# Performance work log

Hardware: AMD Instinct MI355X
Metric: run time of the kernel (lower is better)

Reference implementation:

```python
import jax, jax.numpy as jnp
import numpy as np

EPS_BN = 1e-5   # torch BatchNorm1d default eps
EPS_L1 = 1e-9   # offset-attention renorm eps


def batchnorm(x, g, b):
    # training-mode BN over (batch, points) per channel; x: [B, C, N]
    mu = x.mean(axis=(0, 2), keepdims=True)
    var = x.var(axis=(0, 2), keepdims=True)  # biased, matching torch normalization
    return g[None, :, None] * (x - mu) * jax.lax.rsqrt(var + EPS_BN) + b[None, :, None]


def sub_ie(x, Wqk, Wv, bv, Wt, bt, g, b):
    # x: [B, C, N]; Wqk: [C//4, C] (q_conv and k_conv share weights)
    q = jnp.einsum('dc,bcn->bdn', Wqk, x)                    # [B, C/4, N]
    energy = jnp.einsum('bdi,bdj->bij', q, q)                # [B, N, N] symmetric Gram
    att = jax.nn.softmax(energy, axis=-1)                    # softmax over keys (dim=-1)
    att = att / (EPS_L1 + att.sum(axis=1, keepdims=True))    # extra L1 renorm over queries (dim=1)
    v = jnp.einsum('dc,bcn->bdn', Wv, x) + bv[None, :, None]  # [B, C, N]
    x_r = jnp.einsum('bci,bij->bcj', v, att)                 # bmm(x_v, attention)
    y = jnp.einsum('dc,bcn->bdn', Wt, x - x_r) + bt[None, :, None]
    y = jax.nn.relu(batchnorm(y, g, b))
    return x + y


def setup_inputs() -> dict:
    key = jax.random.key(0)
    ks = jax.random.split(key, 8)
    B, Cin, C, N = 8, 64, 128, 2048
    s = lambda k, shape: jax.random.normal(k, shape, jnp.float32) * 0.05
    return {
        'x':   jax.random.normal(ks[0], (B, Cin, N), jnp.float32),
        'W1':  s(ks[1], (64, 64)),
        'g1':  jnp.ones(64, jnp.float32),  'b1': jnp.zeros(64, jnp.float32),
        'W2':  s(ks[2], (C, 64)),
        'g2':  jnp.ones(C, jnp.float32),   'b2': jnp.zeros(C, jnp.float32),
        'Wqk': s(ks[3], (4, C // 4, C)),
        'Wv':  s(ks[4], (4, C, C)),        'bv': jnp.zeros((4, C), jnp.float32),
        'Wt':  s(ks[5], (4, C, C)),        'bt': jnp.zeros((4, C), jnp.float32),
        'gn':  jnp.ones((4, C), jnp.float32), 'bnb': jnp.zeros((4, C), jnp.float32),
    }


def reference(x, W1, g1, b1, W2, g2, b2, Wqk, Wv, bv, Wt, bt, gn, bnb):
    h = jax.nn.relu(batchnorm(jnp.einsum('dc,bcn->bdn', W1, x), g1, b1))   # [B,64,N]
    h = jax.nn.relu(batchnorm(jnp.einsum('dc,bcn->bdn', W2, h), g2, b2))   # [B,128,N]
    outs = []
    for i in range(4):  # 4 structurally chained offset-attention blocks
        h = sub_ie(h, Wqk[i], Wv[i], bv[i], Wt[i], bt[i], gn[i], bnb[i])
        outs.append(h)
    return jnp.concatenate(outs, axis=1)  # [B, 512, N]
```

## Files before the change

### kernel.cpp

```cpp
#include <hip/hip_runtime.h>
#include <cstdint>
#include <cstddef>

#define NPTS 2048
#define NBAT 8

typedef unsigned long long ull;
typedef __attribute__((ext_vector_type(8))) short bf16x8;
typedef __attribute__((ext_vector_type(4))) float f32x4;

__device__ __forceinline__ float4 ld4(const float* p){ return *reinterpret_cast<const float4*>(p); }
__device__ __forceinline__ void st4(float* p, float4 v){ *reinterpret_cast<float4*>(p) = v; }
__device__ __forceinline__ unsigned short f2bf(float f){
    unsigned int u = __float_as_uint(f);
    u += 0x7FFFu + ((u >> 16) & 1u);
    return (unsigned short)(u >> 16);
}
__device__ __forceinline__ float bf2f(unsigned short h){
    return __uint_as_float(((unsigned int)h) << 16);
}

#define BAR_LDS() do { asm volatile("s_waitcnt lgkmcnt(0)" ::: "memory"); \
                       __builtin_amdgcn_s_barrier(); } while (0)

__global__ __launch_bounds__(256) void zero_kernel(float* __restrict__ p)
{
    int i = (blockIdx.x * 256 + threadIdx.x) * 4;
    st4(&p[i], (float4){0.f, 0.f, 0.f, 0.f});
}

__device__ __forceinline__ void bn_finalize(const float* part, int C, int c,
                                            float& mean, float& istd)
{
    float s = 0.f, s2 = 0.f;
    #pragma unroll
    for (int b = 0; b < NBAT; ++b) {
        s  += part[b * C + c];
        s2 += part[NBAT * C + b * C + c];
    }
    const float invn = 1.f / (NBAT * NPTS);
    mean = s * invn;
    float var = s2 * invn - mean * mean;
    istd = rsqrtf(var + 1e-5f);
}

template<int CIN, int COUT, int TD, int TN, int MODE, bool BIAS, bool BNIN, bool STATS>
__global__ __launch_bounds__(256) void lin_mfma_kernel(
        const float* __restrict__ W, const float* __restrict__ X,
        const float* __restrict__ bias,
        const float* __restrict__ gin, const float* __restrict__ betain,
        const float* __restrict__ pin, float* __restrict__ pout,
        void* __restrict__ outv, void* __restrict__ outv2)
{
    constexpr int WD  = TD / 16;
    constexpr int NPW = TN * WD / 4;
    constexpr int FB  = NPW / 16;
    constexpr int KS  = CIN / 32;
    __shared__ unsigned short Xhi[TN * CIN];
    __shared__ unsigned short Xlo[TN * CIN];
    __shared__ float gaL[CIN];
    __shared__ float beL[CIN];
    const int tid = threadIdx.x;
    const int lane = tid & 63;
    const int w = tid >> 6;
    const int g = lane >> 4;
    const int l15 = lane & 15;
    const int b = blockIdx.z;
    const int d0 = blockIdx.y * TD;
    const int n0 = blockIdx.x * TN;
    const int dw = (w % WD) * 16;
    const int nw = (w / WD) * NPW;

    if (BNIN) {
        if (tid < CIN) {
            float mean, is;
            bn_finalize(pin, CIN, tid, mean, is);
            float ga = gin[tid] * is;
            gaL[tid] = ga;
            beL[tid] = betain[tid] - mean * ga;
        }
        __syncthreads();
    }

    bf16x8 Whi[KS], Wlo[KS];
    {
        const int d = d0 + dw + l15;
        #pragma unroll
        for (int ks = 0; ks < KS; ++ks) {
            float4 a = ld4(&W[(size_t)d * CIN + ks * 32 + g * 8]);
            float4 bq = ld4(&W[(size_t)d * CIN + ks * 32 + g * 8 + 4]);
            float vv[8] = {a.x, a.y, a.z, a.w, bq.x, bq.y, bq.z, bq.w};
            bf16x8 h8, l8;
            #pragma unroll
            for (int e = 0; e < 8; ++e) {
                unsigned short hh = f2bf(vv[e]);
                h8[e] = (short)hh;
                l8[e] = (short)f2bf(vv[e] - bf2f(hh));
            }
            Whi[ks] = h8; Wlo[ks] = l8;
        }
    }
    constexpr int TN4 = TN / 4;
    constexpr int NF = (TN * CIN) / 1024;
    #pragma unroll
    for (int f = 0; f < NF; ++f) {
        int idx = tid + 256 * f;
        int c = idx / TN4;
        int n = (idx % TN4) * 4;
        float4 xv = ld4(&X[((size_t)(b * CIN + c)) * NPTS + n0 + n]);
        float vv[4] = {xv.x, xv.y, xv.z, xv.w};
        if (BNIN) {
            float ga = gaL[c], be = beL[c];
            #pragma unroll
            for (int j2 = 0; j2 < 4; ++j2) vv[j2] = fmaxf(fmaf(ga, vv[j2], be), 0.f);
        }
        #pragma unroll
        for (int j2 = 0; j2 < 4; ++j2) {
            int nn = n + j2;
            int cp = (c + nn * 8) & (CIN - 1);
            unsigned short hh = f2bf(vv[j2]);
            Xhi[nn * CIN + cp] = hh;
            Xlo[nn * CIN + cp] = f2bf(vv[j2] - bf2f(hh));
        }
    }
    __syncthreads();

    f32x4 acc[FB];
    #pragma unroll
    for (int fb = 0; fb < FB; ++fb) acc[fb] = (f32x4){0.f, 0.f, 0.f, 0.f};
    #pragma unroll
    for (int ks = 0; ks < KS; ++ks) {
        #pragma unroll
        for (int fb = 0; fb < FB; ++fb) {
            int n = nw + fb * 16 + l15;
            int cp = (ks * 32 + g * 8 + n * 8) & (CIN - 1);
            bf16x8 xh = *reinterpret_cast<bf16x8*>(&Xhi[n * CIN + cp]);
            bf16x8 xl = *reinterpret_cast<bf16x8*>(&Xlo[n * CIN + cp]);
            acc[fb] = __builtin_amdgcn_mfma_f32_16x16x32_bf16(Wlo[ks], xh, acc[fb], 0, 0, 0);
            acc[fb] = __builtin_amdgcn_mfma_f32_16x16x32_bf16(Whi[ks], xl, acc[fb], 0, 0, 0);
            acc[fb] = __builtin_amdgcn_mfma_f32_16x16x32_bf16(Whi[ks], xh, acc[fb], 0, 0, 0);
        }
    }
    const int dbase = d0 + dw + g * 4;
    float bb[4] = {0.f, 0.f, 0.f, 0.f};
    if (BIAS) {
        float4 b4 = ld4(&bias[dbase]);
        bb[0] = b4.x; bb[1] = b4.y; bb[2] = b4.z; bb[3] = b4.w;
    }
    float s1[4] = {0.f, 0.f, 0.f, 0.f};
    float s2[4] = {0.f, 0.f, 0.f, 0.f};
    #pragma unroll
    for (int fb = 0; fb < FB; ++fb) {
        int ncol = n0 + nw + fb * 16 + l15;
        if (MODE == 2) {
            unsigned short* qh = (unsigned short*)outv;
            unsigned short* ql = (unsigned short*)outv2;
            ushort4 hh, ll;
            float q0 = acc[fb][0], q1 = acc[fb][1], q2 = acc[fb][2], q3 = acc[fb][3];
            hh.x = f2bf(q0); ll.x = f2bf(q0 - bf2f(hh.x));
            hh.y = f2bf(q1); ll.y = f2bf(q1 - bf2f(hh.y));
            hh.z = f2bf(q2); ll.z = f2bf(q2 - bf2f(hh.z));
            hh.w = f2bf(q3); ll.w = f2bf(q3 - bf2f(hh.w));
            *reinterpret_cast<ushort4*>(&qh[((size_t)b * NPTS + ncol) * 32 + dbase]) = hh;
            *reinterpret_cast<ushort4*>(&ql[((size_t)b * NPTS + ncol) * 32 + dbase]) = ll;
        } else if (MODE == 1) {
            unsigned short* ob = (unsigned short*)outv;
            #pragma unroll
            for (int r = 0; r < 4; ++r)
                ob[((size_t)(b * COUT + dbase + r)) * NPTS + ncol] = f2bf(acc[fb][r] + bb[r]);
        } else {
            float* ob = (float*)outv;
            #pragma unroll
            for (int r = 0; r < 4; ++r) {
                float val = acc[fb][r] + bb[r];
                ob[((size_t)(b * COUT + dbase + r)) * NPTS + ncol] = val;
                if (STATS) { s1[r] += val; s2[r] += val * val; }
            }
        }
    }
    if (STATS) {
        #pragma unroll
        for (int r = 0; r < 4; ++r) {
            float a1 = s1[r], a2 = s2[r];
            a1 += __shfl_xor(a1, 1, 64);  a2 += __shfl_xor(a2, 1, 64);
            a1 += __shfl_xor(a1, 2, 64);  a2 += __shfl_xor(a2, 2, 64);
            a1 += __shfl_xor(a1, 4, 64);  a2 += __shfl_xor(a2, 4, 64);
            a1 += __shfl_xor(a1, 8, 64);  a2 += __shfl_xor(a2, 8, 64);
            if (l15 == 0) {
                atomicAdd(&pout[b * COUT + dbase + r], a1);
                atomicAdd(&pout[NBAT * COUT + b * COUT + dbase + r], a2);
            }
        }
    }
}

__global__ __launch_bounds__(256) void rowstats_fused_kernel(
        const unsigned short* __restrict__ qThi, const unsigned short* __restrict__ qTlo,
        float* __restrict__ rowm, float* __restrict__ rowinv)
{
    __shared__ float pm[4][32];
    __shared__ float ps[4][32];
    const int tid = threadIdx.x;
    const int lane = tid & 63;
    const int w = tid >> 6;
    const int b = blockIdx.y;
    const int i0 = blockIdx.x * 32;
    const int g = lane >> 4;
    const int l15 = lane & 15;
    const bf16x8 b0h = *reinterpret_cast<const bf16x8*>(&qThi[((size_t)b * NPTS + i0 + l15) * 32 + g * 8]);
    const bf16x8 b0l = *reinterpret_cast<const bf16x8*>(&qTlo[((size_t)b * NPTS + i0 + l15) * 32 + g * 8]);
    const bf16x8 b1h = *reinterpret_cast<const bf16x8*>(&qThi[((size_t)b * NPTS + i0 + 16 + l15) * 32 + g * 8]);
    const bf16x8 b1l = *reinterpret_cast<const bf16x8*>(&qTlo[((size_t)b * NPTS + i0 + 16 + l15) * 32 + g * 8]);
    float m0 = -1e30f, s0 = 0.f, m1 = -1e30f, s1 = 0.f;
    for (int t = w * 32; t < w * 32 + 32; ++t) {
        int jr = t * 16 + l15;
        const bf16x8 ahi = *reinterpret_cast<const bf16x8*>(&qThi[((size_t)b * NPTS + jr) * 32 + g * 8]);
        const bf16x8 alo = *reinterpret_cast<const bf16x8*>(&qTlo[((size_t)b * NPTS + jr) * 32 + g * 8]);
        f32x4 e0 = {0.f, 0.f, 0.f, 0.f};
        e0 = __builtin_amdgcn_mfma_f32_16x16x32_bf16(alo, b0h, e0, 0, 0, 0);
        e0 = __builtin_amdgcn_mfma_f32_16x16x32_bf16(ahi, b0l, e0, 0, 0, 0);
        e0 = __builtin_amdgcn_mfma_f32_16x16x32_bf16(ahi, b0h, e0, 0, 0, 0);
        f32x4 e1 = {0.f, 0.f, 0.f, 0.f};
        e1 = __builtin_amdgcn_mfma_f32_16x16x32_bf16(alo, b1h, e1, 0, 0, 0);
        e1 = __builtin_amdgcn_mfma_f32_16x16x32_bf16(ahi, b1l, e1, 0, 0, 0);
        e1 = __builtin_amdgcn_mfma_f32_16x16x32_bf16(ahi, b1h, e1, 0, 0, 0);
        float tm0 = fmaxf(fmaxf(e0[0], e0[1]), fmaxf(e0[2], e0[3]));
        float nm0 = fmaxf(m0, tm0);
        s0 *= __expf(m0 - nm0);
        m0 = nm0;
        s0 += __expf(e0[0] - m0) + __expf(e0[1] - m0) + __expf(e0[2] - m0) + __expf(e0[3] - m0);
        float tm1 = fmaxf(fmaxf(e1[0], e1[1]), fmaxf(e1[2], e1[3]));
        float nm1 = fmaxf(m1, tm1);
        s1 *= __expf(m1 - nm1);
        m1 = nm1;
        s1 += __expf(e1[0] - m1) + __expf(e1[1] - m1) + __expf(e1[2] - m1) + __expf(e1[3] - m1);
    }
    #pragma unroll
    for (int o = 16; o <= 32; o <<= 1) {
        float om = __shfl_xor(m0, o, 64);
        float os = __shfl_xor(s0, o, 64);
        float nm = fmaxf(m0, om);
        s0 = s0 * __expf(m0 - nm) + os * __expf(om - nm);
        m0 = nm;
        om = __shfl_xor(m1, o, 64);
        os = __shfl_xor(s1, o, 64);
        nm = fmaxf(m1, om);
        s1 = s1 * __expf(m1 - nm) + os * __expf(om - nm);
        m1 = nm;
    }
    if (lane < 16) {
        pm[w][l15] = m0; ps[w][l15] = s0;
        pm[w][16 + l15] = m1; ps[w][16 + l15] = s1;
    }
    __syncthreads();
    if (tid < 32) {
        float ma = pm[0][tid], mb = pm[1][tid], mc = pm[2][tid], md = pm[3][tid];
        float mf = fmaxf(fmaxf(ma, mb), fmaxf(mc, md));
        float sf = ps[0][tid] * __expf(ma - mf) + ps[1][tid] * __expf(mb - mf)
                 + ps[2][tid] * __expf(mc - mf) + ps[3][tid] * __expf(md - mf);
        rowm[(size_t)b * NPTS + i0 + tid] = mf;
        rowinv[(size_t)b * NPTS + i0 + tid] = 1.f / sf;
    }
}

__global__ __launch_bounds__(512) void attn_fused_kernel(
        const unsigned short* __restrict__ qThi, const unsigned short* __restrict__ qTlo,
        const unsigned short* __restrict__ V,
        const float* __restrict__ rowm, const float* __restrict__ rowinv,
        const float* __restrict__ H, float* __restrict__ T)
{
    __shared__ unsigned short Alds[2][128 * 64];
    __shared__ unsigned short Blds[2][32 * 64];
    __shared__ float cparts[8][16];
    const int tid = threadIdx.x;
    const int b  = blockIdx.y;
    const int j0 = blockIdx.x * 32;
    const int lane = tid & 63;
    const int w = tid >> 6;
    const int g = lane >> 4;
    const int l15 = lane & 15;
    const int jsub = w & 1;
    const int tE = w >> 1;
    const int jl = jsub * 16 + l15;
    const int cb = (w >> 1) * 32;
    const int jb = jsub * 16;
    const int vc = tid >> 3, vslot = tid & 7;
    const int vc1 = (tid + 512) >> 3, vslot1 = (tid + 512) & 7;
    const bf16x8 bhi = *reinterpret_cast<const bf16x8*>(&qThi[((size_t)b * NPTS + j0 + jl) * 32 + g * 8]);
    const bf16x8 blo = *reinterpret_cast<const bf16x8*>(&qTlo[((size_t)b * NPTS + j0 + jl) * 32 + g * 8]);
    f32x4 acc[2];
    acc[0] = (f32x4){0.f, 0.f, 0.f, 0.f};
    acc[1] = (f32x4){0.f, 0.f, 0.f, 0.f};
    float csum = 0.f;

    float4 vreg0 = ld4((const float*)(V + ((size_t)(b * 128 + vc)) * NPTS + vslot * 8));
    float4 vreg1 = ld4((const float*)(V + ((size_t)(b * 128 + vc1)) * NPTS + vslot1 * 8));
    bf16x8 pahi = *reinterpret_cast<const bf16x8*>(&qThi[((size_t)b * NPTS + tE * 16 + l15) * 32 + g * 8]);
    bf16x8 palo = *reinterpret_cast<const bf16x8*>(&qTlo[((size_t)b * NPTS + tE * 16 + l15) * 32 + g * 8]);
    float4 pmv = ld4(&rowm[(size_t)b * NPTS + tE * 16 + g * 4]);
    float4 psv = ld4(&rowinv[(size_t)b * NPTS + tE * 16 + g * 4]);

    int p = 0;
    for (int i0 = 0; i0 < NPTS; i0 += 64) {
        {
            int sl = vslot ^ (vc & 7);
            *reinterpret_cast<float4*>(&Alds[p][vc * 64 + sl * 8]) = vreg0;
            sl = vslot1 ^ (vc1 & 7);
            *reinterpret_cast<float4*>(&Alds[p][vc1 * 64 + sl * 8]) = vreg1;
        }
        {
            f32x4 e4 = {0.f, 0.f, 0.f, 0.f};
            __builtin_amdgcn_s_setprio(1);
            e4 = __builtin_amdgcn_mfma_f32_16x16x32_bf16(palo, bhi, e4, 0, 0, 0);
            e4 = __builtin_amdgcn_mfma_f32_16x16x32_bf16(pahi, blo, e4, 0, 0, 0);
            e4 = __builtin_amdgcn_mfma_f32_16x16x32_bf16(pahi, bhi, e4, 0, 0, 0);
            __builtin_amdgcn_s_setprio(0);
            float p0 = __expf(e4[0] - pmv.x) * psv.x;
            float p1 = __expf(e4[1] - pmv.y) * psv.y;
            float p2 = __expf(e4[2] - pmv.z) * psv.z;
            float p3 = __expf(e4[3] - pmv.w) * psv.w;
            csum += p0 + p1 + p2 + p3;
            int il = tE * 16 + g * 4;
            int sl = (il >> 3) ^ (jl & 7);
            ull pk = (ull)f2bf(p0) | ((ull)f2bf(p1) << 16) |
                     ((ull)f2bf(p2) << 32) | ((ull)f2bf(p3) << 48);
            *reinterpret_cast<ull*>(&Blds[p][jl * 64 + sl * 8 + (il & 7)]) = pk;
        }
        {
            int i0n = (i0 + 64) & (NPTS - 1);
            vreg0 = ld4((const float*)(V + ((size_t)(b * 128 + vc)) * NPTS + i0n + vslot * 8));
            vreg1 = ld4((const float*)(V + ((size_t)(b * 128 + vc1)) * NPTS + i0n + vslot1 * 8));
            pahi = *reinterpret_cast<const bf16x8*>(&qThi[((size_t)b * NPTS + i0n + tE * 16 + l15) * 32 + g * 8]);
            palo = *reinterpret_cast<const bf16x8*>(&qTlo[((size_t)b * NPTS + i0n + tE * 16 + l15) * 32 + g * 8]);
            pmv = ld4(&rowm[(size_t)b * NPTS + i0n + tE * 16 + g * 4]);
            psv = ld4(&rowinv[(size_t)b * NPTS + i0n + tE * 16 + g * 4]);
        }
        BAR_LDS();
        __builtin_amdgcn_s_setprio(1);
        #pragma unroll
        for (int ks = 0; ks < 2; ++ks) {
            int j = jb + l15;
            int slb = (ks * 4 + g) ^ (j & 7);
            bf16x8 bfr = *reinterpret_cast<bf16x8*>(&Blds[p][j * 64 + slb * 8]);
            #pragma unroll
            for (int fa = 0; fa < 2; ++fa) {
                int c = cb + fa * 16 + l15;
                int sla = (ks * 4 + g) ^ (c & 7);
                bf16x8 afr = *reinterpret_cast<bf16x8*>(&Alds[p][c * 64 + sla * 8]);
                acc[fa] = __builtin_amdgcn_mfma_f32_16x16x32_bf16(afr, bfr, acc[fa], 0, 0, 0);
            }
        }
        __builtin_amdgcn_s_setprio(0);
        p ^= 1;
    }
    csum += __shfl_xor(csum, 16, 64);
    csum += __shfl_xor(csum, 32, 64);
    if (lane < 16) cparts[w][l15] = csum;
    __syncthreads();
    float cs = cparts[jsub][l15] + cparts[jsub + 2][l15]
             + cparts[jsub + 4][l15] + cparts[jsub + 6][l15];
    float inv = 1.f / (1e-9f + cs);
    int jg_ = j0 + jb + l15;
    #pragma unroll
    for (int fa = 0; fa < 2; ++fa) {
        #pragma unroll
        for (int r = 0; r < 4; ++r) {
            int c = cb + fa * 16 + g * 4 + r;
            size_t base = ((size_t)(b * 128 + c)) * NPTS + jg_;
            T[base] = H[base] - acc[fa][r] * inv;
        }
    }
}

__global__ __launch_bounds__(256) void bn_apply_kernel(const float* __restrict__ X,
        const float* __restrict__ g, const float* __restrict__ beta,
        const float* __restrict__ part, int C, float* __restrict__ out)
{
    const int bc = blockIdx.y;
    const int c = bc % C;
    const int n = blockIdx.x * 1024 + threadIdx.x * 4;
    float mean, is;
    bn_finalize(part, C, c, mean, is);
    const float ga = g[c] * is;
    const float be = beta[c] - mean * ga;
    float4 v = ld4(&X[(size_t)bc * NPTS + n]);
    float4 o;
    o.x = fmaxf(fmaf(ga, v.x, be), 0.f);
    o.y = fmaxf(fmaf(ga, v.y, be), 0.f);
    o.z = fmaxf(fmaf(ga, v.z, be), 0.f);
    o.w = fmaxf(fmaf(ga, v.w, be), 0.f);
    st4(&out[(size_t)bc * NPTS + n], o);
}

__global__ __launch_bounds__(256) void bn_res_kernel(const float* __restrict__ Y,
        const float* __restrict__ g, const float* __restrict__ beta,
        const float* __restrict__ part, float* __restrict__ H,
        float* __restrict__ out, int blk)
{
    const int bc = blockIdx.y;
    const int c = bc & 127;
    const int b = bc >> 7;
    const int n = blockIdx.x * 1024 + threadIdx.x * 4;
    float mean, is;
    bn_finalize(part, 128, c, mean, is);
    const float ga = g[c] * is;
    const float be = beta[c] - mean * ga;
    float4 yv = ld4(&Y[(size_t)bc * NPTS + n]);
    float4 hv = ld4(&H[(size_t)bc * NPTS + n]);
    float4 o;
    o.x = hv.x + fmaxf(fmaf(ga, yv.x, be), 0.f);
    o.y = hv.y + fmaxf(fmaf(ga, yv.y, be), 0.f);
    o.z = hv.z + fmaxf(fmaf(ga, yv.z, be), 0.f);
    o.w = hv.w + fmaxf(fmaf(ga, yv.w, be), 0.f);
    st4(&H[(size_t)bc * NPTS + n], o);
    st4(&out[((size_t)(b * 512 + blk * 128 + c)) * NPTS + n], o);
}

extern "C" void kernel_launch(void* const* d_in, const int* in_sizes, int n_in,
                              void* d_out, int out_size, void* d_ws, size_t ws_size,
                              hipStream_t stream)
{
    const float* x   = (const float*)d_in[0];
    const float* W1  = (const float*)d_in[1];
    const float* g1  = (const float*)d_in[2];
    const float* b1  = (const float*)d_in[3];
    const float* W2  = (const float*)d_in[4];
    const float* g2  = (const float*)d_in[5];
    const float* b2  = (const float*)d_in[6];
    const float* Wqk = (const float*)d_in[7];
    const float* Wv  = (const float*)d_in[8];
    const float* bv  = (const float*)d_in[9];
    const float* Wt  = (const float*)d_in[10];
    const float* bt  = (const float*)d_in[11];
    const float* gn  = (const float*)d_in[12];
    const float* bnb = (const float*)d_in[13];
    float* out = (float*)d_out;

    float* ws = (float*)d_ws;
    size_t off = 0;
    auto alloc = [&](size_t n) { float* p = ws + off; off += n; return p; };
    float* h      = alloc((size_t)NBAT * 128 * NPTS);
    float* t      = alloc((size_t)NBAT * 128 * NPTS);
    float* y      = alloc((size_t)NBAT * 128 * NPTS);
    float* y2     = alloc((size_t)NBAT * 128 * NPTS);
    float* part   = alloc(6 * 2 * NBAT * 128);
    float* rowm   = alloc((size_t)NBAT * NPTS);
    float* rowinv = alloc((size_t)NBAT * NPTS);
    unsigned short* vb   = (unsigned short*)alloc((size_t)NBAT * 128 * NPTS / 2);
    unsigned short* qThi = (unsigned short*)alloc((size_t)NBAT * NPTS * 32 / 2);
    unsigned short* qTlo = (unsigned short*)alloc((size_t)NBAT * NPTS * 32 / 2);
    const int PSL = 2 * NBAT * 128;

    zero_kernel<<<12, 256, 0, stream>>>(part);

    lin_mfma_kernel<64, 64, 64, 32, 0, false, false, true>
        <<<dim3(64, 1, NBAT), 256, 0, stream>>>(
        W1, x, nullptr, nullptr, nullptr, nullptr, part + 0 * PSL, y, nullptr);
    lin_mfma_kernel<64, 128, 64, 32, 0, false, true, true>
        <<<dim3(64, 2, NBAT), 256, 0, stream>>>(
        W2, y, nullptr, g1, b1, part + 0 * PSL, part + 1 * PSL, y2, nullptr);
    bn_apply_kernel<<<dim3(2, NBAT * 128), 256, 0, stream>>>(
        y2, g2, b2, part + 1 * PSL, 128, h);

    for (int blk = 0; blk < 4; ++blk) {
        lin_mfma_kernel<128, 32, 32, 32, 2, false, false, false>
            <<<dim3(64, 1, NBAT), 256, 0, stream>>>(
            Wqk + (size_t)blk * 32 * 128, h, nullptr,
            nullptr, nullptr, nullptr, nullptr, qThi, qTlo);
        lin_mfma_kernel<128, 128, 64, 32, 1, true, false, false>
            <<<dim3(64, 2, NBAT), 256, 0, stream>>>(
            Wv + (size_t)blk * 128 * 128, h, bv + blk * 128,
            nullptr, nullptr, nullptr, nullptr, vb, nullptr);
        rowstats_fused_kernel<<<dim3(64, NBAT), 256, 0, stream>>>(qThi, qTlo, rowm, rowinv);
        attn_fused_kernel<<<dim3(64, NBAT), 512, 0, stream>>>(
            qThi, qTlo, vb, rowm, rowinv, h, t);
        lin_mfma_kernel<128, 128, 64, 32, 0, true, false, true>
            <<<dim3(64, 2, NBAT), 256, 0, stream>>>(
            Wt + (size_t)blk * 128 * 128, t, bt + blk * 128,
            nullptr, nullptr, nullptr, part + (2 + blk) * PSL, y, nullptr);
        bn_res_kernel<<<dim3(2, NBAT * 128), 256, 0, stream>>>(
            y, gn + blk * 128, bnb + blk * 128, part + (2 + blk) * PSL, h, out, blk);
    }
}
```

Before: 409.7 us.

## Load V tiles via global_load_lds, widen attention K-step, shrink rowstats tile

```diff
diff --git a/kernel.cpp b/kernel.cpp
--- a/kernel.cpp
+++ b/kernel.cpp
@@ -20,8 +20,11 @@
     return __uint_as_float(((unsigned int)h) << 16);
 }
 
-#define BAR_LDS() do { asm volatile("s_waitcnt lgkmcnt(0)" ::: "memory"); \
-                       __builtin_amdgcn_s_barrier(); } while (0)
+typedef __attribute__((address_space(3))) unsigned int lds_u32;
+typedef __attribute__((address_space(1))) const unsigned int glb_u32;
+__device__ __forceinline__ void gl2lds16(const unsigned short* g, unsigned short* l){
+    __builtin_amdgcn_global_load_lds((glb_u32*)g, (lds_u32*)l, 16, 0, 0);
+}
 
 __global__ __launch_bounds__(256) void zero_kernel(float* __restrict__ p)
 {
@@ -198,68 +201,52 @@
         const unsigned short* __restrict__ qThi, const unsigned short* __restrict__ qTlo,
         float* __restrict__ rowm, float* __restrict__ rowinv)
 {
-    __shared__ float pm[4][32];
-    __shared__ float ps[4][32];
-    const int tid = threadIdx.x;
-    const int lane = tid & 63;
-    const int w = tid >> 6;
+    __shared__ float pm[4][16];
+    __shared__ float ps[4][16];
+    const int lane = threadIdx.x & 63;
+    const int w = threadIdx.x >> 6;
     const int b = blockIdx.y;
-    const int i0 = blockIdx.x * 32;
+    const int i0 = blockIdx.x * 16;
     const int g = lane >> 4;
     const int l15 = lane & 15;
-    const bf16x8 b0h = *reinterpret_cast<const bf16x8*>(&qThi[((size_t)b * NPTS + i0 + l15) * 32 + g * 8]);
-    const bf16x8 b0l = *reinterpret_cast<const bf16x8*>(&qTlo[((size_t)b * NPTS + i0 + l15) * 32 + g * 8]);
-    const bf16x8 b1h = *reinterpret_cast<const bf16x8*>(&qThi[((size_t)b * NPTS + i0 + 16 + l15) * 32 + g * 8]);
-    const bf16x8 b1l = *reinterpret_cast<const bf16x8*>(&qTlo[((size_t)b * NPTS + i0 + 16 + l15) * 32 + g * 8]);
-    float m0 = -1e30f, s0 = 0.f, m1 = -1e30f, s1 = 0.f;
+    const int iR = i0 + l15;
+    const bf16x8 bhi = *reinterpret_cast<const bf16x8*>(&qThi[((size_t)b * NPTS + iR) * 32 + g * 8]);
+    const bf16x8 blo = *reinterpret_cast<const bf16x8*>(&qTlo[((size_t)b * NPTS + iR) * 32 + g * 8]);
+    float m = -1e30f, s = 0.f;
     for (int t = w * 32; t < w * 32 + 32; ++t) {
         int jr = t * 16 + l15;
         const bf16x8 ahi = *reinterpret_cast<const bf16x8*>(&qThi[((size_t)b * NPTS + jr) * 32 + g * 8]);
         const bf16x8 alo = *reinterpret_cast<const bf16x8*>(&qTlo[((size_t)b * NPTS + jr) * 32 + g * 8]);
-        f32x4 e0 = {0.f, 0.f, 0.f, 0.f};
-        e0 = __builtin_amdgcn_mfma_f32_16x16x32_bf16(alo, b0h, e0, 0, 0, 0);
-        e0 = __builtin_amdgcn_mfma_f32_16x16x32_bf16(ahi, b0l, e0, 0, 0, 0);
-        e0 = __builtin_amdgcn_mfma_f32_16x16x32_bf16(ahi, b0h, e0, 0, 0, 0);
-        f32x4 e1 = {0.f, 0.f, 0.f, 0.f};
-        e1 = __builtin_amdgcn_mfma_f32_16x16x32_bf16(alo, b1h, e1, 0, 0, 0);
-        e1 = __builtin_amdgcn_mfma_f32_16x16x32_bf16(ahi, b1l, e1, 0, 0, 0);
-        e1 = __builtin_amdgcn_mfma_f32_16x16x32_bf16(ahi, b1h, e1, 0, 0, 0);
-        float tm0 = fmaxf(fmaxf(e0[0], e0[1]), fmaxf(e0[2], e0[3]));
-        float nm0 = fmaxf(m0, tm0);
-        s0 *= __expf(m0 - nm0);
-        m0 = nm0;
-        s0 += __expf(e0[0] - m0) + __expf(e0[1] - m0) + __expf(e0[2] - m0) + __expf(e0[3] - m0);
-        float tm1 = fmaxf(fmaxf(e1[0], e1[1]), fmaxf(e1[2], e1[3]));
-        float nm1 = fmaxf(m1, tm1);
-        s1 *= __expf(m1 - nm1);
-        m1 = nm1;
-        s1 += __expf(e1[0] - m1) + __expf(e1[1] - m1) + __expf(e1[2] - m1) + __expf(e1[3] - m1);
+        f32x4 e4 = {0.f, 0.f, 0.f, 0.f};
+        e4 = __builtin_amdgcn_mfma_f32_16x16x32_bf16(alo, bhi, e4, 0, 0, 0);
+        e4 = __builtin_amdgcn_mfma_f32_16x16x32_bf16(ahi, blo, e4, 0, 0, 0);
+        e4 = __builtin_amdgcn_mfma_f32_16x16x32_bf16(ahi, bhi, e4, 0, 0, 0);
+        float tm = fmaxf(fmaxf(e4[0], e4[1]), fmaxf(e4[2], e4[3]));
+        float nm = fmaxf(m, tm);
+        s *= __expf(m - nm);
+        m = nm;
+        s += __expf(e4[0] - m) + __expf(e4[1] - m) + __expf(e4[2] - m) + __expf(e4[3] - m);
     }
     #pragma unroll
     for (int o = 16; o <= 32; o <<= 1) {
-        float om = __shfl_xor(m0, o, 64);
-        float os = __shfl_xor(s0, o, 64);
-        float nm = fmaxf(m0, om);
-        s0 = s0 * __expf(m0 - nm) + os * __expf(om - nm);
-        m0 = nm;
-        om = __shfl_xor(m1, o, 64);
-        os = __shfl_xor(s1, o, 64);
-        nm = fmaxf(m1, om);
-        s1 = s1 * __expf(m1 - nm) + os * __expf(om - nm);
-        m1 = nm;
-    }
-    if (lane < 16) {
-        pm[w][l15] = m0; ps[w][l15] = s0;
-        pm[w][16 + l15] = m1; ps[w][16 + l15] = s1;
-    }
+        float om = __shfl_xor(m, o, 64);
+        float os = __shfl_xor(s, o, 64);
+        float nm = fmaxf(m, om);
+        s = s * __expf(m - nm) + os * __expf(om - nm);
+        m = nm;
+    }
+    if (lane < 16) { pm[w][l15] = m; ps[w][l15] = s; }
     __syncthreads();
-    if (tid < 32) {
-        float ma = pm[0][tid], mb = pm[1][tid], mc = pm[2][tid], md = pm[3][tid];
-        float mf = fmaxf(fmaxf(ma, mb), fmaxf(mc, md));
-        float sf = ps[0][tid] * __expf(ma - mf) + ps[1][tid] * __expf(mb - mf)
-                 + ps[2][tid] * __expf(mc - mf) + ps[3][tid] * __expf(md - mf);
-        rowm[(size_t)b * NPTS + i0 + tid] = mf;
-        rowinv[(size_t)b * NPTS + i0 + tid] = 1.f / sf;
+    if (threadIdx.x < 16) {
+        float m0 = pm[0][threadIdx.x], m1 = pm[1][threadIdx.x];
+        float m2 = pm[2][threadIdx.x], m3 = pm[3][threadIdx.x];
+        float mf = fmaxf(fmaxf(m0, m1), fmaxf(m2, m3));
+        float sf = ps[0][threadIdx.x] * __expf(m0 - mf)
+                 + ps[1][threadIdx.x] * __expf(m1 - mf)
+                 + ps[2][threadIdx.x] * __expf(m2 - mf)
+                 + ps[3][threadIdx.x] * __expf(m3 - mf);
+        rowm[(size_t)b * NPTS + i0 + threadIdx.x] = mf;
+        rowinv[(size_t)b * NPTS + i0 + threadIdx.x] = 1.f / sf;
     }
 }
 
@@ -269,8 +256,8 @@
         const float* __restrict__ rowm, const float* __restrict__ rowinv,
         const float* __restrict__ H, float* __restrict__ T)
 {
-    __shared__ unsigned short Alds[2][128 * 64];
-    __shared__ unsigned short Blds[2][32 * 64];
+    __shared__ unsigned short Alds[128 * 128];
+    __shared__ unsigned short Blds[32 * 128];
     __shared__ float cparts[8][16];
     const int tid = threadIdx.x;
     const int b  = blockIdx.y;
@@ -280,12 +267,9 @@
     const int g = lane >> 4;
     const int l15 = lane & 15;
     const int jsub = w & 1;
-    const int tE = w >> 1;
     const int jl = jsub * 16 + l15;
     const int cb = (w >> 1) * 32;
     const int jb = jsub * 16;
-    const int vc = tid >> 3, vslot = tid & 7;
-    const int vc1 = (tid + 512) >> 3, vslot1 = (tid + 512) & 7;
     const bf16x8 bhi = *reinterpret_cast<const bf16x8*>(&qThi[((size_t)b * NPTS + j0 + jl) * 32 + g * 8]);
     const bf16x8 blo = *reinterpret_cast<const bf16x8*>(&qTlo[((size_t)b * NPTS + j0 + jl) * 32 + g * 8]);
     f32x4 acc[2];
@@ -293,65 +277,56 @@
     acc[1] = (f32x4){0.f, 0.f, 0.f, 0.f};
     float csum = 0.f;
 
-    float4 vreg0 = ld4((const float*)(V + ((size_t)(b * 128 + vc)) * NPTS + vslot * 8));
-    float4 vreg1 = ld4((const float*)(V + ((size_t)(b * 128 + vc1)) * NPTS + vslot1 * 8));
-    bf16x8 pahi = *reinterpret_cast<const bf16x8*>(&qThi[((size_t)b * NPTS + tE * 16 + l15) * 32 + g * 8]);
-    bf16x8 palo = *reinterpret_cast<const bf16x8*>(&qTlo[((size_t)b * NPTS + tE * 16 + l15) * 32 + g * 8]);
-    float4 pmv = ld4(&rowm[(size_t)b * NPTS + tE * 16 + g * 4]);
-    float4 psv = ld4(&rowinv[(size_t)b * NPTS + tE * 16 + g * 4]);
-
-    int p = 0;
-    for (int i0 = 0; i0 < NPTS; i0 += 64) {
-        {
-            int sl = vslot ^ (vc & 7);
-            *reinterpret_cast<float4*>(&Alds[p][vc * 64 + sl * 8]) = vreg0;
-            sl = vslot1 ^ (vc1 & 7);
-            *reinterpret_cast<float4*>(&Alds[p][vc1 * 64 + sl * 8]) = vreg1;
-        }
-        {
+    for (int i0 = 0; i0 < NPTS; i0 += 128) {
+        __syncthreads();
+        #pragma unroll
+        for (int t = 0; t < 4; ++t) {
+            int c = w * 16 + t * 4 + g;
+            int s = l15;
+            int slot = (s & 8) | ((s & 7) ^ (c & 7));
+            gl2lds16(V + ((size_t)(b * 128 + c)) * NPTS + i0 + slot * 8,
+                     &Alds[(w * 16 + t * 4) * 128]);
+        }
+        #pragma unroll
+        for (int half = 0; half < 2; ++half) {
+            int it = (w >> 1) + half * 4;
+            int iA = i0 + it * 16 + l15;
+            const bf16x8 ahi = *reinterpret_cast<const bf16x8*>(&qThi[((size_t)b * NPTS + iA) * 32 + g * 8]);
+            const bf16x8 alo = *reinterpret_cast<const bf16x8*>(&qTlo[((size_t)b * NPTS + iA) * 32 + g * 8]);
             f32x4 e4 = {0.f, 0.f, 0.f, 0.f};
-            __builtin_amdgcn_s_setprio(1);
-            e4 = __builtin_amdgcn_mfma_f32_16x16x32_bf16(palo, bhi, e4, 0, 0, 0);
-            e4 = __builtin_amdgcn_mfma_f32_16x16x32_bf16(pahi, blo, e4, 0, 0, 0);
-            e4 = __builtin_amdgcn_mfma_f32_16x16x32_bf16(pahi, bhi, e4, 0, 0, 0);
-            __builtin_amdgcn_s_setprio(0);
-            float p0 = __expf(e4[0] - pmv.x) * psv.x;
-            float p1 = __expf(e4[1] - pmv.y) * psv.y;
-            float p2 = __expf(e4[2] - pmv.z) * psv.z;
-            float p3 = __expf(e4[3] - pmv.w) * psv.w;
+            e4 = __builtin_amdgcn_mfma_f32_16x16x32_bf16(alo, bhi, e4, 0, 0, 0);
+            e4 = __builtin_amdgcn_mfma_f32_16x16x32_bf16(ahi, blo, e4, 0, 0, 0);
+            e4 = __builtin_amdgcn_mfma_f32_16x16x32_bf16(ahi, bhi, e4, 0, 0, 0);
+            int ibase = i0 + it * 16 + g * 4;
+            float4 mv = ld4(&rowm[(size_t)b * NPTS + ibase]);
+            float4 sv = ld4(&rowinv[(size_t)b * NPTS + ibase]);
+            float p0 = __expf(e4[0] - mv.x) * sv.x;
+            float p1 = __expf(e4[1] - mv.y) * sv.y;
+            float p2 = __expf(e4[2] - mv.z) * sv.z;
+            float p3 = __expf(e4[3] - mv.w) * sv.w;
             csum += p0 + p1 + p2 + p3;
-            int il = tE * 16 + g * 4;
-            int sl = (il >> 3) ^ (jl & 7);
+            int il = it * 16 + g * 4;
+            int slot = il >> 3;
+            int sl = (slot & 8) | ((slot & 7) ^ (jl & 7));
             ull pk = (ull)f2bf(p0) | ((ull)f2bf(p1) << 16) |
                      ((ull)f2bf(p2) << 32) | ((ull)f2bf(p3) << 48);
-            *reinterpret_cast<ull*>(&Blds[p][jl * 64 + sl * 8 + (il & 7)]) = pk;
-        }
-        {
-            int i0n = (i0 + 64) & (NPTS - 1);
-            vreg0 = ld4((const float*)(V + ((size_t)(b * 128 + vc)) * NPTS + i0n + vslot * 8));
-            vreg1 = ld4((const float*)(V + ((size_t)(b * 128 + vc1)) * NPTS + i0n + vslot1 * 8));
-            pahi = *reinterpret_cast<const bf16x8*>(&qThi[((size_t)b * NPTS + i0n + tE * 16 + l15) * 32 + g * 8]);
-            palo = *reinterpret_cast<const bf16x8*>(&qTlo[((size_t)b * NPTS + i0n + tE * 16 + l15) * 32 + g * 8]);
-            pmv = ld4(&rowm[(size_t)b * NPTS + i0n + tE * 16 + g * 4]);
-            psv = ld4(&rowinv[(size_t)b * NPTS + i0n + tE * 16 + g * 4]);
-        }
-        BAR_LDS();
-        __builtin_amdgcn_s_setprio(1);
-        #pragma unroll
-        for (int ks = 0; ks < 2; ++ks) {
+            *reinterpret_cast<ull*>(&Blds[jl * 128 + sl * 8 + (il & 7)]) = pk;
+        }
+        __syncthreads();
+        #pragma unroll
+        for (int ks = 0; ks < 4; ++ks) {
             int j = jb + l15;
-            int slb = (ks * 4 + g) ^ (j & 7);
-            bf16x8 bfr = *reinterpret_cast<bf16x8*>(&Blds[p][j * 64 + slb * 8]);
+            int slot = ks * 4 + g;
+            int slb = (slot & 8) | ((slot & 7) ^ (j & 7));
+            bf16x8 bfr = *reinterpret_cast<bf16x8*>(&Blds[j * 128 + slb * 8]);
             #pragma unroll
             for (int fa = 0; fa < 2; ++fa) {
                 int c = cb + fa * 16 + l15;
-                int sla = (ks * 4 + g) ^ (c & 7);
-                bf16x8 afr = *reinterpret_cast<bf16x8*>(&Alds[p][c * 64 + sla * 8]);
+                int sla = (slot & 8) | ((slot & 7) ^ (c & 7));
+                bf16x8 afr = *reinterpret_cast<bf16x8*>(&Alds[c * 128 + sla * 8]);
                 acc[fa] = __builtin_amdgcn_mfma_f32_16x16x32_bf16(afr, bfr, acc[fa], 0, 0, 0);
             }
         }
-        __builtin_amdgcn_s_setprio(0);
-        p ^= 1;
     }
     csum += __shfl_xor(csum, 16, 64);
     csum += __shfl_xor(csum, 32, 64);
@@ -471,7 +446,7 @@
             <<<dim3(64, 2, NBAT), 256, 0, stream>>>(
             Wv + (size_t)blk * 128 * 128, h, bv + blk * 128,
             nullptr, nullptr, nullptr, nullptr, vb, nullptr);
-        rowstats_fused_kernel<<<dim3(64, NBAT), 256, 0, stream>>>(qThi, qTlo, rowm, rowinv);
+        rowstats_fused_kernel<<<dim3(128, NBAT), 256, 0, stream>>>(qThi, qTlo, rowm, rowinv);
         attn_fused_kernel<<<dim3(64, NBAT), 512, 0, stream>>>(
             qThi, qTlo, vb, rowm, rowinv, h, t);
         lin_mfma_kernel<128, 128, 64, 32, 0, true, false, true>
```

Result: slower. 445.3 us (+8.7%).
